# Kernel optimization log

Measured on AMD Instinct MI355X. Metric: run time of the kernel, lower is better.

## Reference

```python
import jax, jax.numpy as jnp
import numpy as np

N = 131072        # batch of spacetime points
IN_FEAT = 5       # modified spherical features
WIDTH = 128       # SmoothMLP width (config default)
DEPTH = 4         # hidden layers (config default); 1 input layer + 3 stacked hidden
CLIP = 1.0
EPS = 1e-8


def _init_mlp(key, in_dim, width, n_stack):
    ks = jax.random.split(key, 2 * (n_stack + 2))
    s_in = 1.0 / np.sqrt(in_dim)
    s_h = 1.0 / np.sqrt(width)
    W0 = jax.random.normal(ks[0], (in_dim, width), jnp.float32) * s_in
    b0 = jnp.zeros((width,), jnp.float32)
    Wh = jax.random.normal(ks[1], (n_stack, width, width), jnp.float32) * s_h
    bh = jnp.zeros((n_stack, width), jnp.float32)
    Wo = jax.random.normal(ks[2], (width, 1), jnp.float32) * s_h
    bo = jnp.zeros((1,), jnp.float32)
    return W0, b0, Wh, bh, Wo, bo


def setup_inputs() -> dict:
    key = jax.random.key(0)
    k_x, k_dp, k_ic = jax.random.split(key, 3)
    tx_cart = jax.random.normal(k_x, (N, 4), jnp.float32)
    # make times positive so the integration interval [0, t] is well posed
    tx_cart = tx_cart.at[:, 0].set(jnp.abs(tx_cart[:, 0]) + 0.1)
    dp = _init_mlp(k_dp, IN_FEAT + 1, WIDTH, DEPTH - 1)  # delta_phi net: [t, sph...]
    ic = _init_mlp(k_ic, IN_FEAT, WIDTH, DEPTH - 1)       # initial correction net
    names_dp = ["dp_W0", "dp_b0", "dp_Wh", "dp_bh", "dp_Wo", "dp_bo"]
    names_ic = ["ic_W0", "ic_b0", "ic_Wh", "ic_bh", "ic_Wo", "ic_bo"]
    out = {"tx_cart": tx_cart}
    out.update(dict(zip(names_dp, dp)))
    out.update(dict(zip(names_ic, ic)))
    return out


def _mlp(x, W0, b0, Wh, bh, Wo, bo):
    # SmoothMLP: tanh activations, scalar output. x: (..., in_dim)
    h = jnp.tanh(x @ W0 + b0)
    for i in range(Wh.shape[0]):  # fixed small layer count
        h = jnp.tanh(h @ Wh[i] + bh[i])
    return h @ Wo + bo  # (..., 1)


def _cart_to_mod_sph(x_cart):
    # Modified spherical coords with smooth radial compactification (clip):
    # [r/(clip+r), cos(theta), sin(theta), cos(phi), sin(phi)] -> 5 features
    x, y, z = x_cart[:, 0], x_cart[:, 1], x_cart[:, 2]
    r = jnp.sqrt(x * x + y * y + z * z + EPS)
    rho = jnp.sqrt(x * x + y * y + EPS)
    u = r / (CLIP + r)
    cos_t = z / r
    sin_t = rho / r
    cos_p = x / rho
    sin_p = y / rho
    return jnp.stack([u, cos_t, sin_t, cos_p, sin_p], axis=1)  # (N, 5)


# 3-point Gauss-Legendre nodes/weights on [-1, 1]
_GL_NODES = jnp.array([-np.sqrt(3.0 / 5.0), 0.0, np.sqrt(3.0 / 5.0)], jnp.float32)
_GL_WEIGHTS = jnp.array([5.0 / 9.0, 8.0 / 9.0, 5.0 / 9.0], jnp.float32)


def reference(tx_cart, dp_W0, dp_b0, dp_Wh, dp_bh, dp_Wo, dp_bo,
              ic_W0, ic_b0, ic_Wh, ic_bh, ic_Wo, ic_bo):
    t0 = 0.0
    t = tx_cart[:, 0]                        # (N,) per-row end time
    x_sph = _cart_to_mod_sph(tx_cart[:, 1:4])  # (N, 5)

    # initial correction at t0
    phi0 = _mlp(x_sph, ic_W0, ic_b0, ic_Wh, ic_bh, ic_Wo, ic_bo)[:, 0]  # (N,)

    # GL3 quadrature of d(phi)/dt over [t0, t] per row, fully vectorized
    a = (t - t0) * 0.5                       # (N,) half-width
    b = (t + t0) * 0.5                       # (N,) midpoint
    ts = a[:, None] * _GL_NODES[None, :] + b[:, None]          # (N, 3)
    sph_b = jnp.broadcast_to(x_sph[:, None, :], (x_sph.shape[0], 3, IN_FEAT))
    z = jnp.concatenate([ts[:, :, None], sph_b], axis=2)       # (N, 3, 6)
    vals = _mlp(z, dp_W0, dp_b0, dp_Wh, dp_bh, dp_Wo, dp_bo)[..., 0]  # (N, 3)
    delta_phi = a * jnp.sum(_GL_WEIGHTS * vals, axis=1)        # (N,)

    potential = phi0 + delta_phi
    return potential
```

## Files before the change

### kernel.cpp

```cpp
#include <hip/hip_runtime.h>

#define NPTS 131072

#define FRAG0_OFF    0
#define FRAG0_BYTES  4096
#define FRAGH_OFF    4096
#define HLAYER_BYTES 32768
#define FRAGH_BYTES  (3 * HLAYER_BYTES)
#define BIAS_OFF     (FRAGH_OFF + FRAGH_BYTES)
#define BIAS_BYTES   2048
#define WO_OFF       (BIAS_OFF + BIAS_BYTES)
#define WOBO_BYTES   528
#define MLP_BYTES    (WO_OFF + WOBO_BYTES)

typedef _Float16 f16;
typedef __attribute__((ext_vector_type(8)))  _Float16 f16x8;
typedef __attribute__((ext_vector_type(16))) float    f32x16;

#define C2LOG2E 2.8853900817779268f

__device__ __forceinline__ float tanh2(float x){
  float e = __builtin_amdgcn_exp2f(x);
  return 1.0f - 2.0f * __builtin_amdgcn_rcpf(e + 1.0f);
}

__device__ __forceinline__ void gl_lds16(const void* g, void* l){
  __builtin_amdgcn_global_load_lds(
      (const __attribute__((address_space(1))) void*)g,
      (__attribute__((address_space(3))) void*)l, 16, 0, 0);
}

__global__ void pack_weights(
    const float* __restrict__ dpW0, const float* __restrict__ dpb0,
    const float* __restrict__ dpWh, const float* __restrict__ dpbh,
    const float* __restrict__ dpWo, const float* __restrict__ dpbo,
    const float* __restrict__ icW0, const float* __restrict__ icb0,
    const float* __restrict__ icWh, const float* __restrict__ icbh,
    const float* __restrict__ icWo, const float* __restrict__ icbo,
    unsigned char* __restrict__ ws)
{
  int tid = blockIdx.x * blockDim.x + threadIdx.x;
  int nth = gridDim.x * blockDim.x;
  for (int m = 0; m < 2; ++m){
    const float* W0 = m ? icW0 : dpW0;
    const float* Wh = m ? icWh : dpWh;
    const float* b0 = m ? icb0 : dpb0;
    const float* bh = m ? icbh : dpbh;
    const float* Wo = m ? icWo : dpWo;
    const float* bo = m ? icbo : dpbo;
    const int indim = m ? 5 : 6;
    unsigned char* base = ws + m * MLP_BYTES;

    f16* dstF0 = (f16*)(base + FRAG0_OFF);
    for (int idx = tid; idx < 2048; idx += nth){
      int e    = idx & 7;
      int lane = (idx >> 3) & 63;
      int jt   = idx >> 9;
      int j = 32*jt + (lane & 31);
      int k = 8*(lane >> 5) + e;
      float v = (k < indim) ? W0[k*128 + j] * C2LOG2E : 0.0f;
      dstF0[idx] = (f16)v;
    }
    f16* dstFH = (f16*)(base + FRAGH_OFF);
    for (int idx = tid; idx < 3*16384; idx += nth){
      int layer = idx / 16384;
      int q     = idx & 16383;
      int e    = q & 7;
      int lane = (q >> 3) & 63;
      int f    = q >> 9;
      int jt = f >> 3, s = f & 7;
      int j = 32*jt + (lane & 31);
      int k = 16*s + 8*(lane >> 5) + e;
      int row = (k & ~12) | ((k & 4) << 1) | ((k & 8) >> 1);
      float v = Wh[(layer*128 + row)*128 + j] * C2LOG2E;
      dstFH[idx] = (f16)v;
    }
    float* dstB = (float*)(base + BIAS_OFF);
    for (int idx = tid; idx < 512; idx += nth)
      dstB[idx] = ((idx < 128) ? b0[idx] : bh[idx - 128]) * C2LOG2E;
    float* dstW = (float*)(base + WO_OFF);
    for (int idx = tid; idx < 128; idx += nth) dstW[idx] = Wo[idx];
    if (tid == 0) dstW[128] = bo[0];
  }
}

__device__ __forceinline__ f32x16 load_bias16(const float* bp){
  float4 q0 = *(const float4*)(bp +  0);
  float4 q1 = *(const float4*)(bp +  8);
  float4 q2 = *(const float4*)(bp + 16);
  float4 q3 = *(const float4*)(bp + 24);
  f32x16 a;
  a[0]=q0.x;  a[1]=q0.y;  a[2]=q0.z;  a[3]=q0.w;
  a[4]=q1.x;  a[5]=q1.y;  a[6]=q1.z;  a[7]=q1.w;
  a[8]=q2.x;  a[9]=q2.y;  a[10]=q2.z; a[11]=q2.w;
  a[12]=q3.x; a[13]=q3.y; a[14]=q3.z; a[15]=q3.w;
  return a;
}

#define PIN_V(x) asm("" : "+v"(x))

__global__ __launch_bounds__(256, 2) void node_main(
    const float* __restrict__ tx,
    const unsigned char* __restrict__ ws,
    float* __restrict__ out)
{
  __shared__ __align__(16) unsigned char sHL[2 * 16384];
  __shared__ __align__(16) unsigned char sF0[FRAG0_BYTES];
  __shared__ __align__(16) float sBias[512];
  __shared__ __align__(16) float sWo[136];

  const int tid  = threadIdx.x;
  const int wave = tid >> 6;
  const int lane = tid & 63;
  const int c    = lane & 31;
  const int hi   = lane >> 5;
  const int gp   = blockIdx.x * 128 + wave * 32 + c;

  auto stage_half = [&](const unsigned char* mb, int L, int half, int b){
    const unsigned char* src = mb + FRAGH_OFF + L*HLAYER_BYTES + half*4096;
    unsigned char* dst = sHL + b*16384;
    #pragma unroll
    for (int k = 0; k < 4; ++k){
      int ch = wave + 4*k;
      gl_lds16(src + (ch>>2)*8192 + (ch&3)*1024 + lane*16, dst + ch*1024);
    }
  };
  auto stage_entry = [&](const unsigned char* mb){
    gl_lds16(mb + FRAG0_OFF + wave*1024 + lane*16, sF0 + wave*1024);
    for (int i = tid; i < 128; i += 256)
      ((uint4*)sBias)[i] = ((const uint4*)(mb + BIAS_OFF))[i];
    for (int i = tid; i < 33; i += 256)
      ((uint4*)sWo)[i] = ((const uint4*)(mb + WO_OFF))[i];
    stage_half(mb, 0, 0, 0);
  };

  stage_entry(ws);

  float4 cc = ((const float4*)tx)[gp];
  float x = cc.y, y = cc.z, z = cc.w;
  float xy = x*x + y*y;
  float r    = sqrtf(xy + z*z + 1e-8f);
  float rho  = sqrtf(xy + 1e-8f);
  float rin  = __builtin_amdgcn_rcpf(r);
  float rhin = __builtin_amdgcn_rcpf(rho);
  float u    = r * __builtin_amdgcn_rcpf(1.0f + r);
  float cth  = z * rin;
  float sth  = rho * rin;
  float cph  = x * rhin;
  float sph  = y * rhin;
  float th   = 0.5f * cc.x;

  float vsum = 0.0f;

  auto run_phase = [&](const unsigned char* mb, int c0, int c1){
    f32x16 acc[4];
    union { f16x8 v; unsigned uu[4]; } bf[8];

    #pragma unroll 1
    for (int chain = c0; chain <= c1; ++chain){
      #pragma unroll 1
      for (int L = 0; L < 3; ++L){
        #pragma unroll
        for (int half = 0; half < 2; ++half){
          __syncthreads();
          if (half == 0)           stage_half(mb, L,   1, 1);
          else if (L < 2)          stage_half(mb, L+1, 0, 0);
          else if (chain < c1)     stage_half(mb, 0,   0, 0);

          if (L == 0 && half == 0){
            f16x8 b0f;
            #pragma unroll
            for (int e = 0; e < 8; ++e) b0f[e] = (f16)0.0f;
            if (hi == 0){
              if (chain == 3){
                b0f[0]=(f16)u;   b0f[1]=(f16)cth; b0f[2]=(f16)sth;
                b0f[3]=(f16)cph; b0f[4]=(f16)sph;
              } else {
                const float gn = (chain == 0) ? -0.7745966692414834f :
                                 (chain == 2) ?  0.7745966692414834f : 0.0f;
                float ts = th * (1.0f + gn);
                b0f[0]=(f16)ts;  b0f[1]=(f16)u;   b0f[2]=(f16)cth;
                b0f[3]=(f16)sth; b0f[4]=(f16)cph; b0f[5]=(f16)sph;
              }
            }
            const f16x8* fr = (const f16x8*)sF0;
            #pragma unroll
            for (int jt = 0; jt < 4; ++jt){
              acc[jt] = __builtin_amdgcn_mfma_f32_32x32x16_f16(
                          fr[jt*64 + lane], b0f,
                          load_bias16(&sBias[32*jt + 4*hi]), 0,0,0);
              PIN_V(acc[jt]);
            }
            #pragma unroll
            for (int jt = 0; jt < 4; ++jt)
              #pragma unroll
              for (int cq = 0; cq < 2; ++cq)
                #pragma unroll
                for (int e = 0; e < 4; ++e){
                  float t0 = tanh2(acc[jt][8*cq + 2*e]);
                  float t1 = tanh2(acc[jt][8*cq + 2*e + 1]);
                  auto pk = __builtin_amdgcn_cvt_pkrtz(t0, t1);
                  bf[2*jt + cq].uu[e] = __builtin_bit_cast(unsigned, pk);
                }
          }

          const f16x8* fb = (const f16x8*)(sHL + half*16384);
          #pragma unroll
          for (int jt = 0; jt < 4; ++jt){
            f32x16 t = (half == 0)
                     ? load_bias16(&sBias[(L+1)*128 + 32*jt + 4*hi])
                     : acc[jt];
            #pragma unroll
            for (int s2 = 0; s2 < 4; ++s2)
              t = __builtin_amdgcn_mfma_f32_32x32x16_f16(
                    fb[(jt*4 + s2)*64 + lane], bf[4*half + s2].v, t, 0,0,0);
            PIN_V(t);
            acc[jt] = t;
          }

          if (half == 1){
            if (L < 2){
              #pragma unroll
              for (int jt = 0; jt < 4; ++jt)
                #pragma unroll
                for (int cq = 0; cq < 2; ++cq)
                  #pragma unroll
                  for (int e = 0; e < 4; ++e){
                    float t0 = tanh2(acc[jt][8*cq + 2*e]);
                    float t1 = tanh2(acc[jt][8*cq + 2*e + 1]);
                    auto pk = __builtin_amdgcn_cvt_pkrtz(t0, t1);
                    bf[2*jt + cq].uu[e] = __builtin_bit_cast(unsigned, pk);
                  }
            } else {
              float v = 0.0f;
              #pragma unroll
              for (int jt = 0; jt < 4; ++jt){
                const float* wp = &sWo[32*jt + 4*hi];
                float4 q0 = *(const float4*)(wp +  0);
                float4 q1 = *(const float4*)(wp +  8);
                float4 q2 = *(const float4*)(wp + 16);
                float4 q3 = *(const float4*)(wp + 24);
                f32x16 A = acc[jt];
                v += tanh2(A[0])*q0.x  + tanh2(A[1])*q0.y
                   + tanh2(A[2])*q0.z  + tanh2(A[3])*q0.w
                   + tanh2(A[4])*q1.x  + tanh2(A[5])*q1.y
                   + tanh2(A[6])*q1.z  + tanh2(A[7])*q1.w
                   + tanh2(A[8])*q2.x  + tanh2(A[9])*q2.y
                   + tanh2(A[10])*q2.z + tanh2(A[11])*q2.w
                   + tanh2(A[12])*q3.x + tanh2(A[13])*q3.y
                   + tanh2(A[14])*q3.z + tanh2(A[15])*q3.w;
              }
              v += __shfl_xor(v, 32);
              v += sWo[128];
              if (chain == 3) vsum += v;
              else {
                const float wq = (chain == 1) ? 0.8888888888888889f
                                              : 0.5555555555555556f;
                vsum = __builtin_fmaf(th * wq, v, vsum);
              }
            }
          }
        }
      }
    }
  };

  run_phase(ws, 0, 2);
  __syncthreads();
  stage_entry(ws + MLP_BYTES);
  run_phase(ws + MLP_BYTES, 3, 3);

  if (hi == 0) out[gp] = vsum;
}

extern "C" void kernel_launch(void* const* d_in, const int* in_sizes, int n_in,
                              void* d_out, int out_size, void* d_ws, size_t ws_size,
                              hipStream_t stream)
{
  const float* tx = (const float*)d_in[0];
  pack_weights<<<64, 256, 0, stream>>>(
      (const float*)d_in[1],  (const float*)d_in[2],  (const float*)d_in[3],
      (const float*)d_in[4],  (const float*)d_in[5],  (const float*)d_in[6],
      (const float*)d_in[7],  (const float*)d_in[8],  (const float*)d_in[9],
      (const float*)d_in[10], (const float*)d_in[11], (const float*)d_in[12],
      (unsigned char*)d_ws);
  node_main<<<NPTS/128, 256, 0, stream>>>(tx, (const unsigned char*)d_ws, (float*)d_out);
}
```

Before: 92.44 us.

## Keep first hidden layer resident in LDS and widen blocks to 512 threads

Blocks grow to 8 waves covering 256 points each. The first hidden layer's full weight fragments now stay resident in a dedicated LDS buffer. The remaining hidden layers are staged whole, one layer at a time, instead of in half-layer double-buffered steps. This cuts per-layer staging traffic and the number of block barriers per chain, at the cost of more LDS per block and less overlap between staging and MFMA work. The empty asm register pins are also removed.

After: 88.58 us. -4.2%, faster.

```diff
diff --git a/kernel.cpp b/kernel.cpp
--- a/kernel.cpp
+++ b/kernel.cpp
@@ -97,15 +97,14 @@
   return a;
 }
 
-#define PIN_V(x) asm("" : "+v"(x))
-
-__global__ __launch_bounds__(256, 2) void node_main(
+__global__ __launch_bounds__(512, 2) void node_main(
     const float* __restrict__ tx,
     const unsigned char* __restrict__ ws,
     float* __restrict__ out)
 {
+  __shared__ __align__(16) unsigned char sF0[FRAG0_BYTES];
+  __shared__ __align__(16) unsigned char sL1[HLAYER_BYTES];
   __shared__ __align__(16) unsigned char sHL[2 * 16384];
-  __shared__ __align__(16) unsigned char sF0[FRAG0_BYTES];
   __shared__ __align__(16) float sBias[512];
   __shared__ __align__(16) float sWo[136];
 
@@ -114,24 +113,31 @@
   const int lane = tid & 63;
   const int c    = lane & 31;
   const int hi   = lane >> 5;
-  const int gp   = blockIdx.x * 128 + wave * 32 + c;
+  const int gp   = blockIdx.x * 256 + wave * 32 + c;
 
   auto stage_half = [&](const unsigned char* mb, int L, int half, int b){
     const unsigned char* src = mb + FRAGH_OFF + L*HLAYER_BYTES + half*4096;
     unsigned char* dst = sHL + b*16384;
     #pragma unroll
-    for (int k = 0; k < 4; ++k){
-      int ch = wave + 4*k;
+    for (int k = 0; k < 2; ++k){
+      int ch = wave + 8*k;
       gl_lds16(src + (ch>>2)*8192 + (ch&3)*1024 + lane*16, dst + ch*1024);
     }
   };
   auto stage_entry = [&](const unsigned char* mb){
-    gl_lds16(mb + FRAG0_OFF + wave*1024 + lane*16, sF0 + wave*1024);
-    for (int i = tid; i < 128; i += 256)
+    if (wave < 4)
+      gl_lds16(mb + FRAG0_OFF + wave*1024 + lane*16, sF0 + wave*1024);
+    #pragma unroll
+    for (int k = 0; k < 4; ++k){
+      int ch = wave + 8*k;
+      gl_lds16(mb + FRAGH_OFF + ch*1024 + lane*16, sL1 + ch*1024);
+    }
+    for (int i = tid; i < 128; i += 512)
       ((uint4*)sBias)[i] = ((const uint4*)(mb + BIAS_OFF))[i];
-    for (int i = tid; i < 33; i += 256)
+    for (int i = tid; i < 33; i += 512)
       ((uint4*)sWo)[i] = ((const uint4*)(mb + WO_OFF))[i];
-    stage_half(mb, 0, 0, 0);
+    stage_half(mb, 1, 0, 0);
+    stage_half(mb, 1, 1, 1);
   };
 
   stage_entry(ws);
@@ -150,125 +156,149 @@
   float sph  = y * rhin;
   float th   = 0.5f * cc.x;
 
+  __syncthreads();
+
   float vsum = 0.0f;
-
-  auto run_phase = [&](const unsigned char* mb, int c0, int c1){
-    f32x16 acc[4];
-    union { f16x8 v; unsigned uu[4]; } bf[8];
-
-    #pragma unroll 1
-    for (int chain = c0; chain <= c1; ++chain){
-      #pragma unroll 1
-      for (int L = 0; L < 3; ++L){
-        #pragma unroll
-        for (int half = 0; half < 2; ++half){
-          __syncthreads();
-          if (half == 0)           stage_half(mb, L,   1, 1);
-          else if (L < 2)          stage_half(mb, L+1, 0, 0);
-          else if (chain < c1)     stage_half(mb, 0,   0, 0);
-
-          if (L == 0 && half == 0){
-            f16x8 b0f;
-            #pragma unroll
-            for (int e = 0; e < 8; ++e) b0f[e] = (f16)0.0f;
-            if (hi == 0){
-              if (chain == 3){
-                b0f[0]=(f16)u;   b0f[1]=(f16)cth; b0f[2]=(f16)sth;
-                b0f[3]=(f16)cph; b0f[4]=(f16)sph;
-              } else {
-                const float gn = (chain == 0) ? -0.7745966692414834f :
-                                 (chain == 2) ?  0.7745966692414834f : 0.0f;
-                float ts = th * (1.0f + gn);
-                b0f[0]=(f16)ts;  b0f[1]=(f16)u;   b0f[2]=(f16)cth;
-                b0f[3]=(f16)sth; b0f[4]=(f16)cph; b0f[5]=(f16)sph;
-              }
-            }
-            const f16x8* fr = (const f16x8*)sF0;
-            #pragma unroll
-            for (int jt = 0; jt < 4; ++jt){
-              acc[jt] = __builtin_amdgcn_mfma_f32_32x32x16_f16(
-                          fr[jt*64 + lane], b0f,
-                          load_bias16(&sBias[32*jt + 4*hi]), 0,0,0);
-              PIN_V(acc[jt]);
-            }
-            #pragma unroll
-            for (int jt = 0; jt < 4; ++jt)
-              #pragma unroll
-              for (int cq = 0; cq < 2; ++cq)
-                #pragma unroll
-                for (int e = 0; e < 4; ++e){
-                  float t0 = tanh2(acc[jt][8*cq + 2*e]);
-                  float t1 = tanh2(acc[jt][8*cq + 2*e + 1]);
-                  auto pk = __builtin_amdgcn_cvt_pkrtz(t0, t1);
-                  bf[2*jt + cq].uu[e] = __builtin_bit_cast(unsigned, pk);
-                }
-          }
-
-          const f16x8* fb = (const f16x8*)(sHL + half*16384);
-          #pragma unroll
-          for (int jt = 0; jt < 4; ++jt){
-            f32x16 t = (half == 0)
-                     ? load_bias16(&sBias[(L+1)*128 + 32*jt + 4*hi])
-                     : acc[jt];
-            #pragma unroll
-            for (int s2 = 0; s2 < 4; ++s2)
-              t = __builtin_amdgcn_mfma_f32_32x32x16_f16(
-                    fb[(jt*4 + s2)*64 + lane], bf[4*half + s2].v, t, 0,0,0);
-            PIN_V(t);
-            acc[jt] = t;
-          }
-
-          if (half == 1){
-            if (L < 2){
-              #pragma unroll
-              for (int jt = 0; jt < 4; ++jt)
-                #pragma unroll
-                for (int cq = 0; cq < 2; ++cq)
-                  #pragma unroll
-                  for (int e = 0; e < 4; ++e){
-                    float t0 = tanh2(acc[jt][8*cq + 2*e]);
-                    float t1 = tanh2(acc[jt][8*cq + 2*e + 1]);
-                    auto pk = __builtin_amdgcn_cvt_pkrtz(t0, t1);
-                    bf[2*jt + cq].uu[e] = __builtin_bit_cast(unsigned, pk);
-                  }
-            } else {
-              float v = 0.0f;
-              #pragma unroll
-              for (int jt = 0; jt < 4; ++jt){
-                const float* wp = &sWo[32*jt + 4*hi];
-                float4 q0 = *(const float4*)(wp +  0);
-                float4 q1 = *(const float4*)(wp +  8);
-                float4 q2 = *(const float4*)(wp + 16);
-                float4 q3 = *(const float4*)(wp + 24);
-                f32x16 A = acc[jt];
-                v += tanh2(A[0])*q0.x  + tanh2(A[1])*q0.y
-                   + tanh2(A[2])*q0.z  + tanh2(A[3])*q0.w
-                   + tanh2(A[4])*q1.x  + tanh2(A[5])*q1.y
-                   + tanh2(A[6])*q1.z  + tanh2(A[7])*q1.w
-                   + tanh2(A[8])*q2.x  + tanh2(A[9])*q2.y
-                   + tanh2(A[10])*q2.z + tanh2(A[11])*q2.w
-                   + tanh2(A[12])*q3.x + tanh2(A[13])*q3.y
-                   + tanh2(A[14])*q3.z + tanh2(A[15])*q3.w;
-              }
-              v += __shfl_xor(v, 32);
-              v += sWo[128];
-              if (chain == 3) vsum += v;
-              else {
-                const float wq = (chain == 1) ? 0.8888888888888889f
-                                              : 0.5555555555555556f;
-                vsum = __builtin_fmaf(th * wq, v, vsum);
-              }
-            }
-          }
+  f32x16 acc[4];
+  union { f16x8 v; unsigned uu[4]; } bf[8];
+
+  auto pack_bf = [&](){
+    #pragma unroll
+    for (int jt = 0; jt < 4; ++jt)
+      #pragma unroll
+      for (int cq = 0; cq < 2; ++cq)
+        #pragma unroll
+        for (int e = 0; e < 4; ++e){
+          float t0 = tanh2(acc[jt][8*cq + 2*e]);
+          float t1 = tanh2(acc[jt][8*cq + 2*e + 1]);
+          auto pk = __builtin_amdgcn_cvt_pkrtz(t0, t1);
+          bf[2*jt + cq].uu[e] = __builtin_bit_cast(unsigned, pk);
         }
-      }
-    }
   };
 
-  run_phase(ws, 0, 2);
-  __syncthreads();
-  stage_entry(ws + MLP_BYTES);
-  run_phase(ws + MLP_BYTES, 3, 3);
+  #pragma unroll 1
+  for (int chain = 0; chain < 4; ++chain){
+    const unsigned char* mb = ws + (chain == 3 ? MLP_BYTES : 0);
+    if (chain == 3) __syncthreads();
+
+    f16x8 b0f;
+    #pragma unroll
+    for (int e = 0; e < 8; ++e) b0f[e] = (f16)0.0f;
+    if (hi == 0){
+      if (chain == 3){
+        b0f[0]=(f16)u;   b0f[1]=(f16)cth; b0f[2]=(f16)sth;
+        b0f[3]=(f16)cph; b0f[4]=(f16)sph;
+      } else {
+        const float gn = (chain == 0) ? -0.7745966692414834f :
+                         (chain == 2) ?  0.7745966692414834f : 0.0f;
+        float ts = th * (1.0f + gn);
+        b0f[0]=(f16)ts;  b0f[1]=(f16)u;   b0f[2]=(f16)cth;
+        b0f[3]=(f16)sth; b0f[4]=(f16)cph; b0f[5]=(f16)sph;
+      }
+    }
+
+    {
+      const f16x8* fr = (const f16x8*)sF0;
+      #pragma unroll
+      for (int jt = 0; jt < 4; ++jt)
+        acc[jt] = __builtin_amdgcn_mfma_f32_32x32x16_f16(
+                    fr[jt*64 + lane], b0f,
+                    load_bias16(&sBias[32*jt + 4*hi]), 0,0,0);
+    }
+    pack_bf();
+
+    {
+      const f16x8* fh = (const f16x8*)sL1;
+      #pragma unroll
+      for (int jt = 0; jt < 4; ++jt){
+        f32x16 t = load_bias16(&sBias[128 + 32*jt + 4*hi]);
+        #pragma unroll
+        for (int s = 0; s < 8; ++s)
+          t = __builtin_amdgcn_mfma_f32_32x32x16_f16(
+                fh[(jt*8 + s)*64 + lane], bf[s].v, t, 0,0,0);
+        acc[jt] = t;
+      }
+    }
+    pack_bf();
+
+    __syncthreads();
+    {
+      const f16x8* f0 = (const f16x8*)(sHL);
+      const f16x8* f1 = (const f16x8*)(sHL + 16384);
+      #pragma unroll
+      for (int jt = 0; jt < 4; ++jt){
+        f32x16 t = load_bias16(&sBias[256 + 32*jt + 4*hi]);
+        #pragma unroll
+        for (int s2 = 0; s2 < 4; ++s2)
+          t = __builtin_amdgcn_mfma_f32_32x32x16_f16(
+                f0[(jt*4 + s2)*64 + lane], bf[s2].v, t, 0,0,0);
+        #pragma unroll
+        for (int s2 = 0; s2 < 4; ++s2)
+          t = __builtin_amdgcn_mfma_f32_32x32x16_f16(
+                f1[(jt*4 + s2)*64 + lane], bf[4 + s2].v, t, 0,0,0);
+        acc[jt] = t;
+      }
+    }
+    __syncthreads();
+    stage_half(mb, 2, 0, 0);
+    stage_half(mb, 2, 1, 1);
+    pack_bf();
+    __syncthreads();
+    {
+      const f16x8* f0 = (const f16x8*)(sHL);
+      const f16x8* f1 = (const f16x8*)(sHL + 16384);
+      #pragma unroll
+      for (int jt = 0; jt < 4; ++jt){
+        f32x16 t = load_bias16(&sBias[384 + 32*jt + 4*hi]);
+        #pragma unroll
+        for (int s2 = 0; s2 < 4; ++s2)
+          t = __builtin_amdgcn_mfma_f32_32x32x16_f16(
+                f0[(jt*4 + s2)*64 + lane], bf[s2].v, t, 0,0,0);
+        #pragma unroll
+        for (int s2 = 0; s2 < 4; ++s2)
+          t = __builtin_amdgcn_mfma_f32_32x32x16_f16(
+                f1[(jt*4 + s2)*64 + lane], bf[4 + s2].v, t, 0,0,0);
+        acc[jt] = t;
+      }
+    }
+
+    {
+      float v = 0.0f;
+      #pragma unroll
+      for (int jt = 0; jt < 4; ++jt){
+        const float* wp = &sWo[32*jt + 4*hi];
+        float4 q0 = *(const float4*)(wp +  0);
+        float4 q1 = *(const float4*)(wp +  8);
+        float4 q2 = *(const float4*)(wp + 16);
+        float4 q3 = *(const float4*)(wp + 24);
+        f32x16 A = acc[jt];
+        v += tanh2(A[0])*q0.x  + tanh2(A[1])*q0.y
+           + tanh2(A[2])*q0.z  + tanh2(A[3])*q0.w
+           + tanh2(A[4])*q1.x  + tanh2(A[5])*q1.y
+           + tanh2(A[6])*q1.z  + tanh2(A[7])*q1.w
+           + tanh2(A[8])*q2.x  + tanh2(A[9])*q2.y
+           + tanh2(A[10])*q2.z + tanh2(A[11])*q2.w
+           + tanh2(A[12])*q3.x + tanh2(A[13])*q3.y
+           + tanh2(A[14])*q3.z + tanh2(A[15])*q3.w;
+      }
+      v += __shfl_xor(v, 32);
+      v += sWo[128];
+      if (chain == 3) vsum += v;
+      else {
+        const float wq = (chain == 1) ? 0.8888888888888889f
+                                      : 0.5555555555555556f;
+        vsum = __builtin_fmaf(th * wq, v, vsum);
+      }
+    }
+
+    __syncthreads();
+    if (chain < 2){
+      stage_half(ws, 1, 0, 0);
+      stage_half(ws, 1, 1, 1);
+    } else if (chain == 2){
+      stage_entry(ws + MLP_BYTES);
+    }
+  }
 
   if (hi == 0) out[gp] = vsum;
 }
@@ -284,5 +314,5 @@
       (const float*)d_in[7],  (const float*)d_in[8],  (const float*)d_in[9],
       (const float*)d_in[10], (const float*)d_in[11], (const float*)d_in[12],
       (unsigned char*)d_ws);
-  node_main<<<NPTS/128, 256, 0, stream>>>(tx, (const unsigned char*)d_ws, (float*)d_out);
-}
+  node_main<<<NPTS/256, 512, 0, stream>>>(tx, (const unsigned char*)d_ws, (float*)d_out);
+}
```
